# Performance work log

Measured on AMD Instinct MI355X. Metric: run time of the kernel, lower is better.

## Reference

```python
import jax, jax.numpy as jnp
import numpy as np


def setup_inputs() -> dict:
    key0 = jax.random.key(0)
    kq, kk, kv = jax.random.split(key0, 3)
    B, S, E = 4, 2048, 1024
    query = jax.random.normal(kq, (B, S, E), dtype=jnp.float32)
    key = jax.random.normal(kk, (B, S, E), dtype=jnp.float32)
    value = jax.random.normal(kv, (B, S, E), dtype=jnp.float32)
    attn_mask = jnp.zeros((B, S, S), dtype=jnp.float32)
    return {"query": query, "key": key, "value": value, "attn_mask": attn_mask}


def reference(query, key, value, attn_mask):
    # qk = Q K^T / sqrt(E) + mask; softmax over last dim; dropout is
    # identity in eval mode (reference baseline); out = attn @ V.
    E = query.shape[-1]
    scale = 1.0 / jnp.sqrt(jnp.asarray(E, dtype=query.dtype))
    qk = jnp.einsum("bqe,bke->bqk", query, key) * scale + attn_mask
    attn = jax.nn.softmax(qk, axis=-1)
    out = jnp.einsum("bqk,bke->bqe", attn, value)
    return out
```

## Files before the change

### kernel.cpp

```cpp
#include <hip/hip_runtime.h>
#include <stdint.h>
#include <math.h>

typedef unsigned short u16;
typedef short bf16x8 __attribute__((ext_vector_type(8)));
typedef unsigned short u16x8 __attribute__((ext_vector_type(8)));
typedef unsigned short u16x4 __attribute__((ext_vector_type(4)));
typedef float f32x4 __attribute__((ext_vector_type(4)));

typedef __attribute__((address_space(1))) const void gvoid;
typedef __attribute__((address_space(3))) void lvoid;

#define LOG2E 1.4426950408889634f

__device__ __forceinline__ float bf2f(u16 u) {
  union { unsigned int i; float f; } v; v.i = ((unsigned int)u) << 16; return v.f;
}
__device__ __forceinline__ u16 f2bf(float f) {
  union { float ff; unsigned int i; } v; v.ff = f;
  unsigned int x = v.i;
  return (u16)((x + 0x7FFFu + ((x >> 16) & 1u)) >> 16);
}

__device__ __forceinline__ int xcd_swz(int o, int nwg) {
  return (o & 7) * (nwg >> 3) + (o >> 3);
}

__global__ __launch_bounds__(256)
void cvt2_f32_bf16(const float* __restrict__ s0, u16* __restrict__ d0,
                   const float* __restrict__ s1, u16* __restrict__ d1, long n)
{
  const long nb = n / 2048;
  const float* src = (blockIdx.x < nb) ? s0 : s1;
  u16* dst         = (blockIdx.x < nb) ? d0 : d1;
  const long bid   = (blockIdx.x < nb) ? blockIdx.x : (blockIdx.x - nb);
  long i = (bid * 256 + threadIdx.x) * 8;
  if (i + 8 > n) return;
  f32x4 a = *(const f32x4*)&src[i];
  f32x4 b = *(const f32x4*)&src[i + 4];
  u16x8 o;
#pragma unroll
  for (int j = 0; j < 4; j++) { o[j] = f2bf(a[j]); o[4 + j] = f2bf(b[j]); }
  *(u16x8*)&dst[i] = o;
}

__global__ __launch_bounds__(256)
void cvt_f32_bf16(const float* __restrict__ src, u16* __restrict__ dst, long n)
{
  long i = ((long)blockIdx.x * 256 + threadIdx.x) * 8;
  if (i + 8 > n) return;
  f32x4 a = *(const f32x4*)&src[i];
  f32x4 b = *(const f32x4*)&src[i + 4];
  u16x8 o;
#pragma unroll
  for (int j = 0; j < 4; j++) { o[j] = f2bf(a[j]); o[4 + j] = f2bf(b[j]); }
  *(u16x8*)&dst[i] = o;
}

__global__ __launch_bounds__(256)
void transcvt_v(const float* __restrict__ V, u16* __restrict__ VT, int S, int E)
{
  __shared__ u16 t[64][72];
  const int b = blockIdx.z;
  const float* Vb = V + (long)b * S * E;
  u16* VTb = VT + (long)b * S * E;
  const int k0 = blockIdx.x * 64, n0 = blockIdx.y * 64;
  const int tid = threadIdx.x;
#pragma unroll
  for (int p = 0; p < 2; p++) {
    int kk = p * 32 + (tid >> 3);
    int nn = (tid & 7) * 8;
    f32x4 a = *(const f32x4*)&Vb[(long)(k0 + kk) * E + n0 + nn];
    f32x4 c = *(const f32x4*)&Vb[(long)(k0 + kk) * E + n0 + nn + 4];
#pragma unroll
    for (int j = 0; j < 4; j++) { t[nn + j][kk] = f2bf(a[j]); t[nn + 4 + j][kk] = f2bf(c[j]); }
  }
  __syncthreads();
#pragma unroll
  for (int p = 0; p < 2; p++) {
    int nn = p * 32 + (tid >> 3);
    int kk = (tid & 7) * 8;
    u16x8 u;
#pragma unroll
    for (int j = 0; j < 8; j++) u[j] = t[nn][kk + j];
    *(u16x8*)&VTb[(long)(n0 + nn) * S + k0 + kk] = u;
  }
}

__global__ __launch_bounds__(512, 1)
void gemm_bt_256(const u16* __restrict__ A, int lda,
                 const u16* __restrict__ B, int ldb, long bBatchStride,
                 u16* __restrict__ C, int ldc,
                 int K, float scale, int S, int nbx)
{
  __shared__ u16 LA[2][256][64];
  __shared__ u16 LB[2][256][64];

  const int tid  = threadIdx.x;
  const int lane = tid & 63;
  const int wave = tid >> 6;
  const int wm   = wave >> 2;
  const int wn   = wave & 3;

  const int wgid = xcd_swz(blockIdx.x, gridDim.x);
  const int by   = wgid / nbx;
  const int bx   = wgid - by * nbx;

  const long gTile = (long)by * 256;
  const int  bidx  = (int)(gTile / S);
  const int  nTile = bx * 256;

  const u16* Ab = A + gTile * (long)lda;
  const u16* Bb = B + (long)bidx * bBatchStride + (long)nTile * ldb;

  const int lm  = lane & 15;
  const int lmx = lm & 7;
  const int l47 = lane >> 4;
  const int srw = lane >> 3;
  const int scg = (((lane & 7) ^ (lane >> 3)) * 8);

  f32x4 acc[8][4];
#pragma unroll
  for (int i = 0; i < 8; i++)
#pragma unroll
    for (int j = 0; j < 4; j++) acc[i][j] = (f32x4){0.f, 0.f, 0.f, 0.f};

  bf16x8 afr[8], bA[4], bB[4];

#define STG_A(buf, T, h)                                                      \
  {                                                                           \
    _Pragma("unroll")                                                         \
    for (int p_ = 0; p_ < 2; p_++) {                                          \
      const int ch_ = wave * 2 + p_;                                          \
      const int rr_ = (h) * 128 + ch_ * 8 + srw;                              \
      __builtin_amdgcn_global_load_lds(                                       \
          (gvoid*)&Ab[(long)rr_ * lda + (T) * 64 + scg],                      \
          (lvoid*)((char*)&LA[0][0][0] + (buf) * 32768 + (h) * 16384 + ch_ * 1024), \
          16, 0, 0);                                                          \
    }                                                                         \
  }
#define STG_B(buf, T, h)                                                      \
  {                                                                           \
    _Pragma("unroll")                                                         \
    for (int p_ = 0; p_ < 2; p_++) {                                          \
      const int ch_ = wave * 2 + p_;                                          \
      const int rr_ = (h) * 128 + ch_ * 8 + srw;                              \
      __builtin_amdgcn_global_load_lds(                                       \
          (gvoid*)&Bb[(long)rr_ * ldb + (T) * 64 + scg],                      \
          (lvoid*)((char*)&LB[0][0][0] + (buf) * 32768 + (h) * 16384 + ch_ * 1024), \
          16, 0, 0);                                                          \
    }                                                                         \
  }
#define LDA_HALF(buf, mh)                                                     \
  {                                                                           \
    _Pragma("unroll")                                                         \
    for (int m_ = 0; m_ < 4; m_++)                                            \
      _Pragma("unroll")                                                       \
      for (int kk_ = 0; kk_ < 2; kk_++)                                       \
        afr[m_ * 2 + kk_] = *(const bf16x8*)&LA[buf][wm * 128 + ((mh) * 4 + m_) * 16 + lm][(((kk_ * 4 + l47) ^ lmx) * 8)]; \
  }
#define LDB_HALF(buf, nh, dst)                                                \
  {                                                                           \
    _Pragma("unroll")                                                         \
    for (int n_ = 0; n_ < 2; n_++)                                            \
      _Pragma("unroll")                                                       \
      for (int kk_ = 0; kk_ < 2; kk_++)                                       \
        dst[n_ * 2 + kk_] = *(const bf16x8*)&LB[buf][wn * 64 + ((nh) * 2 + n_) * 16 + lm][(((kk_ * 4 + l47) ^ lmx) * 8)]; \
  }
#define PH(mh, nh, bp)                                                        \
  {                                                                           \
    __builtin_amdgcn_sched_barrier(0);                                        \
    __builtin_amdgcn_s_barrier();                                             \
    asm volatile("s_waitcnt lgkmcnt(0)" ::: "memory");                        \
    __builtin_amdgcn_sched_barrier(0);                                        \
    __builtin_amdgcn_s_setprio(1);                                            \
    _Pragma("unroll")                                                         \
    for (int m_ = 0; m_ < 4; m_++)                                            \
      _Pragma("unroll")                                                       \
      for (int n_ = 0; n_ < 2; n_++)                                          \
        _Pragma("unroll")                                                     \
        for (int kk_ = 0; kk_ < 2; kk_++)                                     \
          acc[(mh) * 4 + m_][(nh) * 2 + n_] =                                 \
              __builtin_amdgcn_mfma_f32_16x16x32_bf16(                        \
                  afr[m_ * 2 + kk_], bp[n_ * 2 + kk_],                        \
                  acc[(mh) * 4 + m_][(nh) * 2 + n_], 0, 0, 0);                \
    __builtin_amdgcn_s_setprio(0);                                            \
    __builtin_amdgcn_sched_barrier(0);                                        \
    __builtin_amdgcn_s_barrier();                                             \
  }

  const int NT = K >> 6;
  const int NI = NT >> 1;

  STG_A(0, 0, 0); STG_A(0, 0, 1); STG_B(0, 0, 0); STG_B(0, 0, 1);
  STG_A(1, 1, 0); STG_B(1, 1, 0);
  asm volatile("s_waitcnt vmcnt(0)" ::: "memory");
  __builtin_amdgcn_sched_barrier(0);
  __builtin_amdgcn_s_barrier();

  for (int i = 0; i < NI - 1; i++) {
    const int t0 = 2 * i, t1 = t0 + 1;
    LDA_HALF(0, 0); LDB_HALF(0, 0, bA);
    STG_B(1, t1, 1);
    PH(0, 0, bA);
    LDB_HALF(0, 1, bB);
    STG_A(1, t1, 1);
    PH(0, 1, bB);
    LDA_HALF(0, 1);
    STG_A(0, t0 + 2, 0);
    PH(1, 0, bA);
    STG_B(0, t0 + 2, 0);
    asm volatile("s_waitcnt vmcnt(4)" ::: "memory");
    PH(1, 1, bB);
    LDA_HALF(1, 0); LDB_HALF(1, 0, bA);
    STG_B(0, t0 + 2, 1);
    PH(0, 0, bA);
    LDB_HALF(1, 1, bB);
    STG_A(0, t0 + 2, 1);
    PH(0, 1, bB);
    LDA_HALF(1, 1);
    STG_A(1, t1 + 2, 0);
    PH(1, 0, bA);
    STG_B(1, t1 + 2, 0);
    asm volatile("s_waitcnt vmcnt(4)" ::: "memory");
    PH(1, 1, bB);
  }

  {
    const int t1 = NT - 1;
    LDA_HALF(0, 0); LDB_HALF(0, 0, bA);
    STG_B(1, t1, 1);
    PH(0, 0, bA);
    LDB_HALF(0, 1, bB);
    STG_A(1, t1, 1);
    PH(0, 1, bB);
    LDA_HALF(0, 1);
    PH(1, 0, bA);
    asm volatile("s_waitcnt vmcnt(0)" ::: "memory");
    PH(1, 1, bB);
    LDA_HALF(1, 0); LDB_HALF(1, 0, bA);
    PH(0, 0, bA);
    LDB_HALF(1, 1, bB);
    PH(0, 1, bB);
    LDA_HALF(1, 1);
    PH(1, 0, bA);
    PH(1, 1, bB);
  }

  const int lr = (lane >> 4) * 4;
#pragma unroll
  for (int mf = 0; mf < 8; mf++) {
#pragma unroll
    for (int nf = 0; nf < 4; nf++) {
      long gr = gTile + wm * 128 + mf * 16 + lr;
      int  cc = nTile + wn * 64 + nf * 16 + lm;
#pragma unroll
      for (int i2 = 0; i2 < 4; i2++)
        C[(gr + i2) * (long)ldc + cc] = f2bf(acc[mf][nf][i2] * scale);
    }
  }
#undef STG_A
#undef STG_B
#undef LDA_HALF
#undef LDB_HALF
#undef PH
}

__global__ __launch_bounds__(512, 1)
void gemm_pv_256(const u16* __restrict__ A, int lda,
                 const u16* __restrict__ B, int ldb, long bBatchStride,
                 float* __restrict__ C, int ldc,
                 int K, int S, int nbx)
{
  __shared__ u16 LA[2][256][64];
  __shared__ u16 LB[2][128][64];

  const int tid  = threadIdx.x;
  const int lane = tid & 63;
  const int wave = tid >> 6;
  const int wm   = wave >> 1;
  const int wn   = wave & 1;

  const int wgid = xcd_swz(blockIdx.x, gridDim.x);
  const int by   = wgid / nbx;
  const int bx   = wgid - by * nbx;

  const long gTile = (long)by * 256;
  const int  bidx  = (int)(gTile / S);
  const int  nTile = bx * 128;

  const u16* Ab = A + gTile * (long)lda;
  const u16* Bb = B + (long)bidx * bBatchStride + (long)nTile * ldb;

  const int lm  = lane & 15;
  const int lmx = lm & 7;
  const int l47 = lane >> 4;
  const int srw = lane >> 3;
  const int scg = (((lane & 7) ^ (lane >> 3)) * 8);

  f32x4 acc[4][4];
#pragma unroll
  for (int i = 0; i < 4; i++)
#pragma unroll
    for (int j = 0; j < 4; j++) acc[i][j] = (f32x4){0.f, 0.f, 0.f, 0.f};

  bf16x8 afr[4], ball[8];

#define STG_A(buf, T, h)                                                      \
  {                                                                           \
    _Pragma("unroll")                                                         \
    for (int p_ = 0; p_ < 2; p_++) {                                          \
      const int ch_ = wave * 2 + p_;                                          \
      const int rr_ = (h) * 128 + ch_ * 8 + srw;                              \
      __builtin_amdgcn_global_load_lds(                                       \
          (gvoid*)&Ab[(long)rr_ * lda + (T) * 64 + scg],                      \
          (lvoid*)((char*)&LA[0][0][0] + (buf) * 32768 + (h) * 16384 + ch_ * 1024), \
          16, 0, 0);                                                          \
    }                                                                         \
  }
#define STG_B(buf, T, h)                                                      \
  {                                                                           \
    const int rr_ = (h) * 64 + wave * 8 + srw;                                \
    __builtin_amdgcn_global_load_lds(                                         \
        (gvoid*)&Bb[(long)rr_ * ldb + (T) * 64 + scg],                        \
        (lvoid*)((char*)&LB[0][0][0] + (buf) * 16384 + (h) * 8192 + wave * 1024), \
        16, 0, 0);                                                            \
  }
#define LDA_HALF(buf, mh)                                                     \
  {                                                                           \
    _Pragma("unroll")                                                         \
    for (int m_ = 0; m_ < 2; m_++)                                            \
      _Pragma("unroll")                                                       \
      for (int kk_ = 0; kk_ < 2; kk_++)                                       \
        afr[m_ * 2 + kk_] = *(const bf16x8*)&LA[buf][wm * 64 + ((mh) * 2 + m_) * 16 + lm][(((kk_ * 4 + l47) ^ lmx) * 8)]; \
  }
#define LDB_ALL(buf)                                                          \
  {                                                                           \
    _Pragma("unroll")                                                         \
    for (int n_ = 0; n_ < 4; n_++)                                            \
      _Pragma("unroll")                                                       \
      for (int kk_ = 0; kk_ < 2; kk_++)                                       \
        ball[n_ * 2 + kk_] = *(const bf16x8*)&LB[buf][wn * 64 + n_ * 16 + lm][(((kk_ * 4 + l47) ^ lmx) * 8)]; \
  }
#define PH(mh)                                                                \
  {                                                                           \
    __builtin_amdgcn_sched_barrier(0);                                        \
    __builtin_amdgcn_s_barrier();                                             \
    asm volatile("s_waitcnt lgkmcnt(0)" ::: "memory");                        \
    __builtin_amdgcn_sched_barrier(0);                                        \
    __builtin_amdgcn_s_setprio(1);                                            \
    _Pragma("unroll")                                                         \
    for (int m_ = 0; m_ < 2; m_++)                                            \
      _Pragma("unroll")                                                       \
      for (int n_ = 0; n_ < 4; n_++)                                          \
        _Pragma("unroll")                                                     \
        for (int kk_ = 0; kk_ < 2; kk_++)                                     \
          acc[(mh) * 2 + m_][n_] =                                            \
              __builtin_amdgcn_mfma_f32_16x16x32_bf16(                        \
                  afr[m_ * 2 + kk_], ball[n_ * 2 + kk_],                      \
                  acc[(mh) * 2 + m_][n_], 0, 0, 0);                           \
    __builtin_amdgcn_s_setprio(0);                                            \
    __builtin_amdgcn_sched_barrier(0);                                        \
    __builtin_amdgcn_s_barrier();                                             \
  }

  const int NT = K >> 6;
  const int NI = NT >> 1;

  STG_A(0, 0, 0); STG_A(0, 0, 1); STG_B(0, 0, 0); STG_B(0, 0, 1);
  STG_A(1, 1, 0); STG_B(1, 1, 0);
  asm volatile("s_waitcnt vmcnt(0)" ::: "memory");
  __builtin_amdgcn_sched_barrier(0);
  __builtin_amdgcn_s_barrier();

  for (int i = 0; i < NI - 1; i++) {
    const int t0 = 2 * i, t1 = t0 + 1;
    LDA_HALF(0, 0); LDB_ALL(0);
    STG_B(1, t1, 1);
    STG_A(1, t1, 1);
    PH(0);
    LDA_HALF(0, 1);
    STG_A(0, t0 + 2, 0);
    STG_B(0, t0 + 2, 0);
    asm volatile("s_waitcnt vmcnt(3)" ::: "memory");
    PH(1);
    LDA_HALF(1, 0); LDB_ALL(1);
    STG_B(0, t0 + 2, 1);
    STG_A(0, t0 + 2, 1);
    PH(0);
    LDA_HALF(1, 1);
    STG_A(1, t1 + 2, 0);
    STG_B(1, t1 + 2, 0);
    asm volatile("s_waitcnt vmcnt(3)" ::: "memory");
    PH(1);
  }

  {
    const int t1 = NT - 1;
    LDA_HALF(0, 0); LDB_ALL(0);
    STG_B(1, t1, 1);
    STG_A(1, t1, 1);
    PH(0);
    LDA_HALF(0, 1);
    asm volatile("s_waitcnt vmcnt(0)" ::: "memory");
    PH(1);
    LDA_HALF(1, 0); LDB_ALL(1);
    PH(0);
    LDA_HALF(1, 1);
    PH(1);
  }

  const int lr = (lane >> 4) * 4;
#pragma unroll
  for (int mf = 0; mf < 4; mf++) {
#pragma unroll
    for (int nf = 0; nf < 4; nf++) {
      long gr = gTile + wm * 64 + mf * 16 + lr;
      int  cc = nTile + wn * 64 + nf * 16 + lm;
#pragma unroll
      for (int i2 = 0; i2 < 4; i2++)
        C[(gr + i2) * (long)ldc + cc] = acc[mf][nf][i2];
    }
  }
#undef STG_A
#undef STG_B
#undef LDA_HALF
#undef LDB_ALL
#undef PH
}

template<int HASMASK, int COUT>
__global__ __launch_bounds__(256, 3)
void gemm_bt_fast(const u16* __restrict__ A, int lda, long aRowOff,
                  const u16* __restrict__ B, int ldb, long bBatchStride,
                  void* __restrict__ Cp, int ldc, long cRowOff,
                  const float* __restrict__ maskf,
                  int K, float scale, long g0, int S)
{
  const int tid  = threadIdx.x;
  const int lane = tid & 63;
  const int wave = tid >> 6;
  const long gTile = g0 + (long)blockIdx.y * 128;
  const int  bidx  = (int)(gTile / S);
  const int  nTile = blockIdx.x * 128;

  __shared__ u16 As[128][32];
  __shared__ u16 Bs[128][32];

  const u16* Ab = A + (gTile - aRowOff) * (long)lda;
  const u16* Bb = B + (long)bidx * bBatchStride + (long)nTile * ldb;

  const int qm = (wave >> 1) * 64;
  const int qn = (wave & 1) * 64;
  const int lm  = lane & 15;
  const int lkB = (lane >> 4) * 16;

  const int sr = lane >> 2;
  const int sc = (lane & 3) * 8;

  f32x4 acc[4][4];
#pragma unroll
  for (int i = 0; i < 4; i++)
#pragma unroll
    for (int j = 0; j < 4; j++) acc[i][j] = (f32x4){0.f, 0.f, 0.f, 0.f};

  for (int k0 = 0; k0 < K; k0 += 32) {
#pragma unroll
    for (int p = 0; p < 2; p++) {
      const int chunk = wave * 2 + p;
      const int r = chunk * 16 + sr;
      __builtin_amdgcn_global_load_lds(
          (gvoid*)&Ab[(long)r * lda + k0 + sc],
          (lvoid*)((char*)&As[0][0] + chunk * 1024),
          16, 0, 0);
      __builtin_amdgcn_global_load_lds(
          (gvoid*)&Bb[(long)r * ldb + k0 + sc],
          (lvoid*)((char*)&Bs[0][0] + chunk * 1024),
          16, 0, 0);
    }
    __syncthreads();

    bf16x8 af[4], bfr[4];
#pragma unroll
    for (int rt = 0; rt < 4; rt++)
      af[rt] = *(const bf16x8*)((const char*)&As[qm + rt * 16 + lm][0] + lkB);
#pragma unroll
    for (int ct = 0; ct < 4; ct++)
      bfr[ct] = *(const bf16x8*)((const char*)&Bs[qn + ct * 16 + lm][0] + lkB);

#pragma unroll
    for (int rt = 0; rt < 4; rt++)
#pragma unroll
      for (int ct = 0; ct < 4; ct++)
        acc[rt][ct] = __builtin_amdgcn_mfma_f32_16x16x32_bf16(af[rt], bfr[ct], acc[rt][ct], 0, 0, 0);
    __syncthreads();
  }

  const int lr = (lane >> 4) * 4;
#pragma unroll
  for (int rt = 0; rt < 4; rt++) {
#pragma unroll
    for (int ct = 0; ct < 4; ct++) {
      long gr = gTile + qm + rt * 16 + lr;
      int  cc = nTile + qn + ct * 16 + lm;
#pragma unroll
      for (int i = 0; i < 4; i++) {
        float v = acc[rt][ct][i] * scale;
        if (HASMASK) v += maskf[(gr + i) * (long)ldc + cc];
        if (COUT == 0)
          ((u16*)Cp)[(gr + i - cRowOff) * (long)ldc + cc] = f2bf(v);
        else
          ((float*)Cp)[(gr + i - cRowOff) * (long)ldc + cc] = v;
      }
    }
  }
}

template<int ASRC, int BSRC, int BMODE, int HASMASK, int COUT>
__global__ __launch_bounds__(256, 2)
void gemm_bt(const void* __restrict__ Ap, int lda, long aRowOff,
             const void* __restrict__ Bp, int ldb, long bBatchStride,
             void* __restrict__ Cp, int ldc, long cRowOff,
             const float* __restrict__ maskf,
             int K, float scale, long g0, int S)
{
  const int tid  = threadIdx.x;
  const int lane = tid & 63;
  const int wave = tid >> 6;
  const long gTile = g0 + (long)blockIdx.y * 128;
  const int  b     = (int)(gTile / S);
  const int  nTile = blockIdx.x * 128;

  __shared__ u16 As[128][40];
  __shared__ u16 Bs[128][40];

  const int qm = (wave >> 1) * 64;
  const int qn = (wave & 1) * 64;

  f32x4 acc[4][4];
#pragma unroll
  for (int i = 0; i < 4; i++)
#pragma unroll
    for (int j = 0; j < 4; j++) acc[i][j] = (f32x4){0.f, 0.f, 0.f, 0.f};

  const u16*   Ab = (const u16*)Ap   + (gTile - aRowOff) * (long)lda;
  const float* Af = (const float*)Ap + (gTile - aRowOff) * (long)lda;
  const u16*   Bb = (const u16*)Bp   + (long)b * bBatchStride;
  const float* Bf = (const float*)Bp + (long)b * bBatchStride;

  const int lm = lane & 15;
  const int lk = (lane >> 4) * 8;

  for (int k0 = 0; k0 < K; k0 += 32) {
    if (ASRC == 0) {
      int srow = tid >> 2, scol = (tid & 3) * 8;
#pragma unroll
      for (int p = 0; p < 2; p++) {
        int r = p * 64 + srow;
        *(u16x8*)&As[r][scol] = *(const u16x8*)&Ab[(long)r * lda + k0 + scol];
      }
    } else {
      int srow = tid >> 3, scol = (tid & 7) * 4;
#pragma unroll
      for (int p = 0; p < 4; p++) {
        int r = p * 32 + srow;
        f32x4 a = *(const f32x4*)&Af[(long)r * lda + k0 + scol];
        u16x4 o;
#pragma unroll
        for (int j = 0; j < 4; j++) o[j] = f2bf(a[j]);
        *(u16x4*)&As[r][scol] = o;
      }
    }
    if (BMODE == 0) {
      if (BSRC == 0) {
        int srow = tid >> 2, scol = (tid & 3) * 8;
#pragma unroll
        for (int p = 0; p < 2; p++) {
          int r = p * 64 + srow;
          *(u16x8*)&Bs[r][scol] = *(const u16x8*)&Bb[(long)(nTile + r) * ldb + k0 + scol];
        }
      } else {
        int srow = tid >> 3, scol = (tid & 7) * 4;
#pragma unroll
        for (int p = 0; p < 4; p++) {
          int r = p * 32 + srow;
          f32x4 a = *(const f32x4*)&Bf[(long)(nTile + r) * ldb + k0 + scol];
          u16x4 o;
#pragma unroll
          for (int j = 0; j < 4; j++) o[j] = f2bf(a[j]);
          *(u16x4*)&Bs[r][scol] = o;
        }
      }
    }
    __syncthreads();

    bf16x8 af[4], bfr[4];
#pragma unroll
    for (int rt = 0; rt < 4; rt++)
      af[rt] = *(const bf16x8*)&As[qm + rt * 16 + lm][lk];
    if (BMODE == 0) {
#pragma unroll
      for (int ct = 0; ct < 4; ct++)
        bfr[ct] = *(const bf16x8*)&Bs[qn + ct * 16 + lm][lk];
    } else {
#pragma unroll
      for (int ct = 0; ct < 4; ct++) {
        const float* vp = Bf + (long)(k0 + lk) * ldb + nTile + qn + ct * 16 + lm;
#pragma unroll
        for (int j = 0; j < 8; j++) bfr[ct][j] = (short)f2bf(vp[(long)j * ldb]);
      }
    }
#pragma unroll
    for (int rt = 0; rt < 4; rt++)
#pragma unroll
      for (int ct = 0; ct < 4; ct++)
        acc[rt][ct] = __builtin_amdgcn_mfma_f32_16x16x32_bf16(af[rt], bfr[ct], acc[rt][ct], 0, 0, 0);
    __syncthreads();
  }

  const int lr = (lane >> 4) * 4;
#pragma unroll
  for (int rt = 0; rt < 4; rt++) {
#pragma unroll
    for (int ct = 0; ct < 4; ct++) {
      long gr = gTile + qm + rt * 16 + lr;
      int  cc = nTile + qn + ct * 16 + lm;
#pragma unroll
      for (int i = 0; i < 4; i++) {
        float v = acc[rt][ct][i] * scale;
        if (HASMASK) v += maskf[(gr + i) * (long)ldc + cc];
        if (COUT == 0)
          ((u16*)Cp)[(gr + i - cRowOff) * (long)ldc + cc] = f2bf(v);
        else
          ((float*)Cp)[(gr + i - cRowOff) * (long)ldc + cc] = v;
      }
    }
  }
}

__global__ __launch_bounds__(256)
void softmax_rows_wave(u16* __restrict__ Sbuf, const float* __restrict__ maskf,
                       int ncols)
{
  const int wave = threadIdx.x >> 6;
  const int lane = threadIdx.x & 63;
  const long row = (long)blockIdx.x * 4 + wave;
  u16* rp = Sbuf + row * (long)ncols;
  const float* mp = maskf + row * (long)ncols;

  float x[32];
  float m = -3.0e38f;
#pragma unroll
  for (int j = 0; j < 4; j++) {
    const int c = j * 512 + lane * 8;
    u16x8 u = *(const u16x8*)&rp[c];
    f32x4 ma = *(const f32x4*)&mp[c];
    f32x4 mb = *(const f32x4*)&mp[c + 4];
#pragma unroll
    for (int i = 0; i < 4; i++) {
      x[j * 8 + i]     = bf2f(u[i])     + ma[i];
      x[j * 8 + 4 + i] = bf2f(u[4 + i]) + mb[i];
    }
#pragma unroll
    for (int i = 0; i < 8; i++) m = fmaxf(m, x[j * 8 + i]);
  }
#pragma unroll
  for (int off = 32; off; off >>= 1) m = fmaxf(m, __shfl_xor(m, off, 64));

  float s = 0.f;
#pragma unroll
  for (int i = 0; i < 32; i++) { x[i] = exp2f((x[i] - m) * LOG2E); s += x[i]; }
#pragma unroll
  for (int off = 32; off; off >>= 1) s += __shfl_xor(s, off, 64);
  const float inv = 1.0f / s;

#pragma unroll
  for (int j = 0; j < 4; j++) {
    const int c = j * 512 + lane * 8;
    u16x8 o;
#pragma unroll
    for (int i = 0; i < 8; i++) o[i] = f2bf(x[j * 8 + i] * inv);
    *(u16x8*)&rp[c] = o;
  }
}

template<int HASM>
__global__ __launch_bounds__(256)
void softmax_rows(u16* __restrict__ Sbuf, const float* __restrict__ maskf, int ncols)
{
  const long row = blockIdx.x;
  u16* rp = Sbuf + row * (long)ncols;
  const int tid = threadIdx.x;

  u16x8 u = *(const u16x8*)&rp[tid * 8];
  float x[8];
  if (HASM) {
    const float* mp = maskf + row * (long)ncols + tid * 8;
    f32x4 ma = *(const f32x4*)&mp[0];
    f32x4 mb = *(const f32x4*)&mp[4];
#pragma unroll
    for (int i = 0; i < 4; i++) { x[i] = bf2f(u[i]) + ma[i]; x[4 + i] = bf2f(u[4 + i]) + mb[i]; }
  } else {
#pragma unroll
    for (int i = 0; i < 8; i++) x[i] = bf2f(u[i]);
  }
  float m = -3.0e38f;
#pragma unroll
  for (int i = 0; i < 8; i++) m = fmaxf(m, x[i]);
#pragma unroll
  for (int off = 32; off; off >>= 1) m = fmaxf(m, __shfl_xor(m, off, 64));
  __shared__ float redm[4];
  if ((tid & 63) == 0) redm[tid >> 6] = m;
  __syncthreads();
  m = fmaxf(fmaxf(redm[0], redm[1]), fmaxf(redm[2], redm[3]));

  float e[8];
  float s = 0.f;
#pragma unroll
  for (int i = 0; i < 8; i++) { e[i] = exp2f((x[i] - m) * LOG2E); s += e[i]; }
#pragma unroll
  for (int off = 32; off; off >>= 1) s += __shfl_xor(s, off, 64);
  __shared__ float reds[4];
  if ((tid & 63) == 0) reds[tid >> 6] = s;
  __syncthreads();
  s = reds[0] + reds[1] + reds[2] + reds[3];

  float inv = 1.0f / s;
  u16x8 o;
#pragma unroll
  for (int i = 0; i < 8; i++) o[i] = f2bf(e[i] * inv);
  *(u16x8*)&rp[tid * 8] = o;
}

extern "C" void kernel_launch(void* const* d_in, const int* in_sizes, int n_in,
                              void* d_out, int out_size, void* d_ws, size_t ws_size,
                              hipStream_t stream)
{
  const float* Q    = (const float*)d_in[0];
  const float* Km   = (const float*)d_in[1];
  const float* V    = (const float*)d_in[2];
  const float* mask = (const float*)d_in[3];
  float* out = (float*)d_out;

  const long qsz = in_sizes[0];
  const long msz = in_sizes[3];
  const long E = 1024;
  const long S = (msz / qsz) * E;
  const long B = qsz / (S * E);
  const long G = B * S;
  const float scale = 1.0f / sqrtf((float)E);

  const size_t mergedBytes = (size_t)(2 * qsz) * 2 + (size_t)G * S * 2;
  const long nwgQK = (S / 256) * (G / 256);
  const long nwgPV = (E / 128) * (G / 256);
  if (ws_size >= mergedBytes && (S % 512) == 0 && (G % 256) == 0 &&
      (E % 128) == 0 && (nwgQK % 8) == 0 && (nwgPV % 8) == 0) {
    char* w = (char*)d_ws;
    u16* Qb   = (u16*)w;
    u16* Kb   = (u16*)(w + (size_t)qsz * 2);
    u16* Sbuf = (u16*)(w + (size_t)(2 * qsz) * 2);
    u16* VTb  = Qb;

    cvt2_f32_bf16<<<dim3((unsigned)(2 * qsz / 2048)), 256, 0, stream>>>(
        Q, Qb, Km, Kb, qsz);

    gemm_bt_256<<<dim3((unsigned)nwgQK), 512, 0, stream>>>(
        Qb, (int)E, Kb, (int)E, S * E,
        Sbuf, (int)S, (int)E, scale, (int)S, (int)(S / 256));

    softmax_rows_wave<<<dim3((unsigned)(G / 4)), 256, 0, stream>>>(
        Sbuf, mask, (int)S);

    transcvt_v<<<dim3(S / 64, E / 64, B), 256, 0, stream>>>(V, VTb, (int)S, (int)E);

    gemm_pv_256<<<dim3((unsigned)nwgPV), 512, 0, stream>>>(
        Sbuf, (int)S, VTb, (int)S, E * S,
        out, (int)E, (int)S, (int)S, (int)(E / 128));
    return;
  }

  const size_t convBytes = (size_t)(3 * qsz) * 2;
  const size_t rowBytes  = (size_t)S * 2;
  char* w = (char*)d_ws;
  size_t avail = ws_size;
  const bool haveConv = (ws_size >= convBytes + 128 * rowBytes);

  u16 *Qb = nullptr, *Kb = nullptr, *VTb = nullptr;
  if (haveConv) {
    Qb  = (u16*)w;              w += (size_t)qsz * 2;
    Kb  = (u16*)w;              w += (size_t)qsz * 2;
    VTb = (u16*)w;              w += (size_t)qsz * 2;
    avail -= convBytes;
  }
  long Rmax = (long)((avail / rowBytes) / 128) * 128;
  if (Rmax > G) Rmax = G;
  if (Rmax < 128) Rmax = 128;
  u16* Sbuf = (u16*)w;

  if (haveConv) {
    cvt_f32_bf16<<<dim3((unsigned)(qsz / 2048)), 256, 0, stream>>>(Q, Qb, qsz);
    cvt_f32_bf16<<<dim3((unsigned)(qsz / 2048)), 256, 0, stream>>>(Km, Kb, qsz);
    transcvt_v<<<dim3(S / 64, E / 64, B), 256, 0, stream>>>(V, VTb, (int)S, (int)E);
  }

  for (long g0 = 0; g0 < G; g0 += Rmax) {
    const long R = (G - g0 < Rmax) ? (G - g0) : Rmax;
    if (haveConv) {
      gemm_bt_fast<1, 0><<<dim3(S / 128, R / 128), 256, 0, stream>>>(
          Qb, (int)E, 0L, Kb, (int)E, S * E,
          Sbuf, (int)S, g0, mask, (int)E, scale, g0, (int)S);
    } else {
      gemm_bt<1, 1, 0, 1, 0><<<dim3(S / 128, R / 128), 256, 0, stream>>>(
          Q, (int)E, 0L, Km, (int)E, S * E,
          Sbuf, (int)S, g0, mask, (int)E, scale, g0, (int)S);
    }
    softmax_rows<0><<<dim3(R), 256, 0, stream>>>(Sbuf, nullptr, (int)S);
    if (haveConv) {
      gemm_bt_fast<0, 1><<<dim3(E / 128, R / 128), 256, 0, stream>>>(
          Sbuf, (int)S, g0, VTb, (int)S, E * S,
          out, (int)E, 0L, nullptr, (int)S, 1.0f, g0, (int)S);
    } else {
      gemm_bt<0, 1, 1, 0, 1><<<dim3(E / 128, R / 128), 256, 0, stream>>>(
          Sbuf, (int)S, g0, V, (int)E, S * E,
          out, (int)E, 0L, nullptr, (int)S, 1.0f, g0, (int)S);
    }
  }
}
```

Baseline: 263.3 us.

## Triple-buffer LDS tiles in PV GEMM with full-tile prefetch two ahead

```diff
diff --git a/kernel.cpp b/kernel.cpp
--- a/kernel.cpp
+++ b/kernel.cpp
@@ -272,8 +272,8 @@
                  float* __restrict__ C, int ldc,
                  int K, int S, int nbx)
 {
-  __shared__ u16 LA[2][256][64];
-  __shared__ u16 LB[2][128][64];
+  __shared__ u16 LA[3][256][64];
+  __shared__ u16 LB[3][128][64];
 
   const int tid  = threadIdx.x;
   const int lane = tid & 63;
@@ -304,45 +304,42 @@
 #pragma unroll
     for (int j = 0; j < 4; j++) acc[i][j] = (f32x4){0.f, 0.f, 0.f, 0.f};
 
-  bf16x8 afr[4], ball[8];
-
-#define STG_A(buf, T, h)                                                      \
+  bf16x8 afr[8], ball[8];
+
+#define STG_T(buf, T)                                                         \
   {                                                                           \
     _Pragma("unroll")                                                         \
-    for (int p_ = 0; p_ < 2; p_++) {                                          \
-      const int ch_ = wave * 2 + p_;                                          \
-      const int rr_ = (h) * 128 + ch_ * 8 + srw;                              \
+    for (int h_ = 0; h_ < 2; h_++) {                                          \
+      _Pragma("unroll")                                                       \
+      for (int p_ = 0; p_ < 2; p_++) {                                        \
+        const int ch_ = wave * 2 + p_;                                        \
+        const int rr_ = h_ * 128 + ch_ * 8 + srw;                             \
+        __builtin_amdgcn_global_load_lds(                                     \
+            (gvoid*)&Ab[(long)rr_ * lda + (T) * 64 + scg],                    \
+            (lvoid*)((char*)&LA[0][0][0] + (buf) * 32768 + h_ * 16384 + ch_ * 1024), \
+            16, 0, 0);                                                        \
+      }                                                                       \
+      const int rb_ = h_ * 64 + wave * 8 + srw;                               \
       __builtin_amdgcn_global_load_lds(                                       \
-          (gvoid*)&Ab[(long)rr_ * lda + (T) * 64 + scg],                      \
-          (lvoid*)((char*)&LA[0][0][0] + (buf) * 32768 + (h) * 16384 + ch_ * 1024), \
+          (gvoid*)&Bb[(long)rb_ * ldb + (T) * 64 + scg],                      \
+          (lvoid*)((char*)&LB[0][0][0] + (buf) * 16384 + h_ * 8192 + wave * 1024), \
           16, 0, 0);                                                          \
     }                                                                         \
   }
-#define STG_B(buf, T, h)                                                      \
-  {                                                                           \
-    const int rr_ = (h) * 64 + wave * 8 + srw;                                \
-    __builtin_amdgcn_global_load_lds(                                         \
-        (gvoid*)&Bb[(long)rr_ * ldb + (T) * 64 + scg],                        \
-        (lvoid*)((char*)&LB[0][0][0] + (buf) * 16384 + (h) * 8192 + wave * 1024), \
-        16, 0, 0);                                                            \
-  }
-#define LDA_HALF(buf, mh)                                                     \
+#define LD_ALL(buf)                                                           \
   {                                                                           \
     _Pragma("unroll")                                                         \
-    for (int m_ = 0; m_ < 2; m_++)                                            \
+    for (int m_ = 0; m_ < 4; m_++)                                            \
       _Pragma("unroll")                                                       \
       for (int kk_ = 0; kk_ < 2; kk_++)                                       \
-        afr[m_ * 2 + kk_] = *(const bf16x8*)&LA[buf][wm * 64 + ((mh) * 2 + m_) * 16 + lm][(((kk_ * 4 + l47) ^ lmx) * 8)]; \
-  }
-#define LDB_ALL(buf)                                                          \
-  {                                                                           \
+        afr[m_ * 2 + kk_] = *(const bf16x8*)&LA[buf][wm * 64 + m_ * 16 + lm][(((kk_ * 4 + l47) ^ lmx) * 8)]; \
     _Pragma("unroll")                                                         \
     for (int n_ = 0; n_ < 4; n_++)                                            \
       _Pragma("unroll")                                                       \
       for (int kk_ = 0; kk_ < 2; kk_++)                                       \
         ball[n_ * 2 + kk_] = *(const bf16x8*)&LB[buf][wn * 64 + n_ * 16 + lm][(((kk_ * 4 + l47) ^ lmx) * 8)]; \
   }
-#define PH(mh)                                                                \
+#define PH32()                                                                \
   {                                                                           \
     __builtin_amdgcn_sched_barrier(0);                                        \
     __builtin_amdgcn_s_barrier();                                             \
@@ -350,65 +347,45 @@
     __builtin_amdgcn_sched_barrier(0);                                        \
     __builtin_amdgcn_s_setprio(1);                                            \
     _Pragma("unroll")                                                         \
-    for (int m_ = 0; m_ < 2; m_++)                                            \
+    for (int m_ = 0; m_ < 4; m_++)                                            \
       _Pragma("unroll")                                                       \
       for (int n_ = 0; n_ < 4; n_++)                                          \
         _Pragma("unroll")                                                     \
         for (int kk_ = 0; kk_ < 2; kk_++)                                     \
-          acc[(mh) * 2 + m_][n_] =                                            \
-              __builtin_amdgcn_mfma_f32_16x16x32_bf16(                        \
-                  afr[m_ * 2 + kk_], ball[n_ * 2 + kk_],                      \
-                  acc[(mh) * 2 + m_][n_], 0, 0, 0);                           \
+          acc[m_][n_] = __builtin_amdgcn_mfma_f32_16x16x32_bf16(              \
+              afr[m_ * 2 + kk_], ball[n_ * 2 + kk_], acc[m_][n_], 0, 0, 0);   \
     __builtin_amdgcn_s_setprio(0);                                            \
     __builtin_amdgcn_sched_barrier(0);                                        \
     __builtin_amdgcn_s_barrier();                                             \
   }
 
   const int NT = K >> 6;
-  const int NI = NT >> 1;
-
-  STG_A(0, 0, 0); STG_A(0, 0, 1); STG_B(0, 0, 0); STG_B(0, 0, 1);
-  STG_A(1, 1, 0); STG_B(1, 1, 0);
-  asm volatile("s_waitcnt vmcnt(0)" ::: "memory");
+
+  STG_T(0, 0); STG_T(1, 1);
+  asm volatile("s_waitcnt vmcnt(6)" ::: "memory");
   __builtin_amdgcn_sched_barrier(0);
   __builtin_amdgcn_s_barrier();
 
-  for (int i = 0; i < NI - 1; i++) {
-    const int t0 = 2 * i, t1 = t0 + 1;
-    LDA_HALF(0, 0); LDB_ALL(0);
-    STG_B(1, t1, 1);
-    STG_A(1, t1, 1);
-    PH(0);
-    LDA_HALF(0, 1);
-    STG_A(0, t0 + 2, 0);
-    STG_B(0, t0 + 2, 0);
-    asm volatile("s_waitcnt vmcnt(3)" ::: "memory");
-    PH(1);
-    LDA_HALF(1, 0); LDB_ALL(1);
-    STG_B(0, t0 + 2, 1);
-    STG_A(0, t0 + 2, 1);
-    PH(0);
-    LDA_HALF(1, 1);
-    STG_A(1, t1 + 2, 0);
-    STG_B(1, t1 + 2, 0);
-    asm volatile("s_waitcnt vmcnt(3)" ::: "memory");
-    PH(1);
-  }
-
-  {
-    const int t1 = NT - 1;
-    LDA_HALF(0, 0); LDB_ALL(0);
-    STG_B(1, t1, 1);
-    STG_A(1, t1, 1);
-    PH(0);
-    LDA_HALF(0, 1);
-    asm volatile("s_waitcnt vmcnt(0)" ::: "memory");
-    PH(1);
-    LDA_HALF(1, 0); LDB_ALL(1);
-    PH(0);
-    LDA_HALF(1, 1);
-    PH(1);
-  }
+  int t = 0;
+  for (; t + 4 < NT; t += 3) {
+    LD_ALL(0);
+    STG_T(2, t + 2);
+    asm volatile("s_waitcnt vmcnt(6)" ::: "memory");
+    PH32();
+    LD_ALL(1);
+    STG_T(0, t + 3);
+    asm volatile("s_waitcnt vmcnt(6)" ::: "memory");
+    PH32();
+    LD_ALL(2);
+    STG_T(1, t + 4);
+    asm volatile("s_waitcnt vmcnt(6)" ::: "memory");
+    PH32();
+  }
+  LD_ALL(0);
+  asm volatile("s_waitcnt vmcnt(0)" ::: "memory");
+  PH32();
+  LD_ALL(1);
+  PH32();
 
   const int lr = (lane >> 4) * 4;
 #pragma unroll
@@ -422,11 +399,9 @@
         C[(gr + i2) * (long)ldc + cc] = acc[mf][nf][i2];
     }
   }
-#undef STG_A
-#undef STG_B
-#undef LDA_HALF
-#undef LDB_ALL
-#undef PH
+#undef STG_T
+#undef LD_ALL
+#undef PH32
 }
 
 template<int HASMASK, int COUT>
@@ -753,8 +728,10 @@
   const size_t mergedBytes = (size_t)(2 * qsz) * 2 + (size_t)G * S * 2;
   const long nwgQK = (S / 256) * (G / 256);
   const long nwgPV = (E / 128) * (G / 256);
+  const long NTpv  = S / 64;
   if (ws_size >= mergedBytes && (S % 512) == 0 && (G % 256) == 0 &&
-      (E % 128) == 0 && (nwgQK % 8) == 0 && (nwgPV % 8) == 0) {
+      (E % 128) == 0 && (nwgQK % 8) == 0 && (nwgPV % 8) == 0 &&
+      NTpv >= 5 && ((NTpv - 2) % 3) == 0) {
     char* w = (char*)d_ws;
     u16* Qb   = (u16*)w;
     u16* Kb   = (u16*)(w + (size_t)qsz * 2);
```

Result: no change. 264.2 us (+0.3%).
